# Kernel optimization log

Measured on AMD Instinct MI355X. Metric: run time of the kernel, lower is better.

Reference implementation:

```python
import jax, jax.numpy as jnp
import numpy as np

INF = 1e20


def setup_inputs() -> dict:
    key = jax.random.key(0)
    k1, k2, k3 = jax.random.split(key, 3)
    B, Q, M, F, D = 16, 64, 512, 16, 512
    return {
        "query_embed": jax.random.normal(k1, (B, Q, D), dtype=jnp.float32),
        "in_memory_embed": jax.random.normal(k2, (B, M, F, D), dtype=jnp.float32),
        "out_memory_embed": jax.random.normal(k3, (B, M, F, D), dtype=jnp.float32),
        "ctx_mask": jnp.ones((B, M, F), dtype=jnp.float32),
        "query_mask": jnp.ones((B, Q), dtype=jnp.float32),
    }


def reference(query_embed, in_memory_embed, out_memory_embed, ctx_mask, query_mask):
    # co-attention scores: [B, Q, M, F]
    attention = jnp.einsum("bqd,bmfd->bqmf", query_embed, in_memory_embed)
    # additive INF masking (torch: mask*att - (1-mask)*INF)
    cm = ctx_mask[:, None, :, :]            # [B,1,M,F]
    attention = cm * attention - (1.0 - cm) * INF
    qm = query_mask[:, :, None, None]       # [B,Q,1,1]
    attention = qm * attention - (1.0 - qm) * INF
    # NOTE: torch code computes a max-pool over Q for kb_feature_att but
    # immediately overwrites it with softmax of a ones/ctx mask -> dead code.
    mask = ctx_mask * 1.0 - (1.0 - ctx_mask) * INF        # [B,M,F]
    kb_feature_att = jax.nn.softmax(mask, axis=-1)        # [B,M,F]
    # weighted read over feature slots: [B,M,D]
    in_mem = jnp.einsum("bmf,bmfd->bmd", kb_feature_att, in_memory_embed)
    out_mem = out_memory_embed.sum(axis=2)                # [B,M,D]
    # max-pool over feature axis F -> [B,Q,M]
    att_qm = attention.max(axis=-1)
    probs = jax.nn.softmax(att_qm, axis=-1)               # over M
    new_query_embed = query_embed + jnp.einsum("bqm,bmd->bqd", probs, out_mem)
    probs2 = jax.nn.softmax(att_qm, axis=1)               # over Q
    in_mem = in_mem + jnp.einsum("bqm,bqd->bmd", probs2, new_query_embed)
    return (new_query_embed, in_mem, out_mem)
```

## Files before the change

kernel.cpp:

```cpp
#include <hip/hip_runtime.h>

#define INF_F 1e20f
#define B_ 16
#define Q_ 64
#define M_ 512
#define F_ 16
#define D_ 512

typedef __attribute__((ext_vector_type(8))) short short8v;
typedef __attribute__((ext_vector_type(4))) float f32x4;

static __device__ __forceinline__ float bits_f(unsigned u) { return __uint_as_float(u); }

static __device__ __forceinline__ void split4(float4 v, uint2& H, uint2& L) {
    unsigned hx = __float_as_uint(v.x) & 0xffff0000u, hy = __float_as_uint(v.y) & 0xffff0000u;
    unsigned hz = __float_as_uint(v.z) & 0xffff0000u, hw = __float_as_uint(v.w) & 0xffff0000u;
    H.x = (hx >> 16) | hy;
    H.y = (hz >> 16) | hw;
    L.x = (__float_as_uint(v.x - bits_f(hx)) >> 16) | (__float_as_uint(v.y - bits_f(hy)) & 0xffff0000u);
    L.y = (__float_as_uint(v.z - bits_f(hz)) >> 16) | (__float_as_uint(v.w - bits_f(hw)) & 0xffff0000u);
}

__global__ __launch_bounds__(256) void k_q_split(
    const float* __restrict__ q, short8v* __restrict__ qh, short8v* __restrict__ ql)
{
    int u = blockIdx.x * 256 + threadIdx.x;
    int row = u & 63, lg = (u >> 6) & 3, kc = (u >> 8) & 15, b = u >> 12;
    const float4* q4 = (const float4*)q;
    size_t s = (size_t)(b * 64 + row) * 128 + kc * 8 + lg * 2;
    float4 v0 = q4[s], v1 = q4[s + 1];
    uint2 H0, L0, H1, L1;
    split4(v0, H0, L0);
    split4(v1, H1, L1);
    uint4 H = make_uint4(H0.x, H0.y, H1.x, H1.y);
    uint4 L = make_uint4(L0.x, L0.y, L1.x, L1.y);
    *(uint4*)&qh[u] = H;
    *(uint4*)&ql[u] = L;
}

__global__ __launch_bounds__(256) void k_att_mfma(
    const short8v* __restrict__ qh, const short8v* __restrict__ ql,
    const float* __restrict__ in_mem, const float* __restrict__ out_mem,
    const float* __restrict__ ctx_mask, const float* __restrict__ query_mask,
    float* __restrict__ att_qm, float* __restrict__ in_mem_base,
    float* __restrict__ out_mem_sum)
{
    __shared__ __align__(16) short Mh[2][5120];
    __shared__ __align__(16) short Ml[2][5120];

    const int bid = blockIdx.x;
    const int b   = bid & 15;
    const int m0  = (bid >> 4) * 8;
    const int t   = threadIdx.x;
    const int w   = t >> 6;
    const int lane = t & 63;
    const int lr  = lane & 15;
    const int lg  = lane >> 4;
    const int r0  = t >> 3, c0 = t & 7;

    const int tt   = t & 127;
    const int msel = tt >> 4, col4 = (tt >> 1) & 7, half = tt & 1;
    const bool is_in = (t < 128);

    float wj[8];
    if (is_in) {
        const float* cm = ctx_mask + ((size_t)b * M_ + m0 + msel) * F_;
        float wv[16]; float mx = -INF_F;
        #pragma unroll
        for (int f = 0; f < 16; ++f) {
            float c = cm[f];
            float v = c - (1.0f - c) * INF_F;
            wv[f] = v; mx = fmaxf(mx, v);
        }
        float sum = 0.f;
        #pragma unroll
        for (int f = 0; f < 16; ++f) { wv[f] = __expf(wv[f] - mx); sum += wv[f]; }
        float inv = 1.0f / sum;
        #pragma unroll
        for (int j = 0; j < 8; ++j) wj[j] = wv[half * 8 + j] * inv;
    } else {
        #pragma unroll
        for (int j = 0; j < 8; ++j) wj[j] = 1.0f;
    }

    const float4* in4 = (const float4*)in_mem;
    const float4* ot4 = (const float4*)out_mem;
    const size_t mb    = (size_t)((b * M_ + m0) * F_) * 128;
    const float4* fsrc = is_in ? in4 : ot4;
    float4* fdst       = is_in ? (float4*)in_mem_base : (float4*)out_mem_sum;
    const size_t fbase = (size_t)((b * M_ + m0 + msel) * F_ + half * 8) * 128 + col4;
    const size_t fob   = (size_t)(b * M_ + m0 + msel) * 128 + col4;
    const int qbase0   = b * 16 * 256 + lg * 64 + lr;

    f32x4 acc[2][4];
    #pragma unroll
    for (int i = 0; i < 2; ++i)
        #pragma unroll
        for (int j = 0; j < 4; ++j) acc[i][j] = (f32x4){0, 0, 0, 0};

    float4 stg[4], fv[8];
    short8v qfh[4], qfl[4];

    #pragma unroll
    for (int i = 0; i < 4; ++i) stg[i] = in4[mb + (size_t)(r0 + i * 32) * 128 + c0];
    #pragma unroll
    for (int j = 0; j < 8; ++j) fv[j] = fsrc[fbase + (size_t)j * 128];
    #pragma unroll
    for (int tq = 0; tq < 4; ++tq) { qfh[tq] = qh[qbase0 + tq * 16]; qfl[tq] = ql[qbase0 + tq * 16]; }

#define BODY(kc_, bi_) do {                                                      \
                                              \
        _Pragma("unroll")                                                        \
        for (int i = 0; i < 4; ++i) {                                            \
            int r = r0 + i * 32;                                                 \
            uint2 H, L; split4(stg[i], H, L);                                    \
            int off = r * 40 + (((c0 >> 1) ^ ((r & 1) << 1)) << 3) + ((c0 & 1) << 2); \
            *(uint2*)&Mh[bi_][off] = H;                                          \
            *(uint2*)&Ml[bi_][off] = L;                                          \
        }                                                                        \
        if ((kc_) < 15) {                                                        \
            _Pragma("unroll")                                                    \
            for (int i = 0; i < 4; ++i)                                          \
                stg[i] = in4[mb + (size_t)(r0 + i * 32) * 128 + ((kc_) + 1) * 8 + c0]; \
        }                                                                        \
        asm volatile("s_waitcnt lgkmcnt(0)" ::: "memory");                       \
        __builtin_amdgcn_s_barrier();                                            \
                                                 \
        _Pragma("unroll")                                                        \
        for (int tm = 0; tm < 2; ++tm) {                                         \
            int row = (2 * w + tm) * 16 + lr;                                    \
            int off = row * 40 + ((lg ^ ((row & 1) << 1)) << 3);                 \
            short8v bh = *(const short8v*)&Mh[bi_][off];                         \
            short8v bl = *(const short8v*)&Ml[bi_][off];                         \
            _Pragma("unroll")                                                    \
            for (int tq = 0; tq < 4; ++tq) {                                     \
                acc[tm][tq] = __builtin_amdgcn_mfma_f32_16x16x32_bf16(qfh[tq], bh, acc[tm][tq], 0, 0, 0); \
                acc[tm][tq] = __builtin_amdgcn_mfma_f32_16x16x32_bf16(qfh[tq], bl, acc[tm][tq], 0, 0, 0); \
                acc[tm][tq] = __builtin_amdgcn_mfma_f32_16x16x32_bf16(qfl[tq], bh, acc[tm][tq], 0, 0, 0); \
            }                                                                    \
        }                                                                        \
        if ((kc_) < 15) {                                                        \
            int qb = qbase0 + ((kc_) + 1) * 256;                                 \
            _Pragma("unroll")                                                    \
            for (int tq = 0; tq < 4; ++tq) { qfh[tq] = qh[qb + tq * 16]; qfl[tq] = ql[qb + tq * 16]; } \
        }                                                                        \
                                                           \
        {                                                                        \
            float4 s = make_float4(0, 0, 0, 0);                                  \
            _Pragma("unroll")                                                    \
            for (int j = 0; j < 8; ++j) {                                        \
                s.x += wj[j] * fv[j].x; s.y += wj[j] * fv[j].y;                  \
                s.z += wj[j] * fv[j].z; s.w += wj[j] * fv[j].w;                  \
            }                                                                    \
            if ((kc_) < 15) {                                                    \
                _Pragma("unroll")                                                \
                for (int j = 0; j < 8; ++j)                                      \
                    fv[j] = fsrc[fbase + (size_t)j * 128 + ((kc_) + 1) * 8];     \
            }                                                                    \
            s.x += __shfl_xor(s.x, 1, 64); s.y += __shfl_xor(s.y, 1, 64);        \
            s.z += __shfl_xor(s.z, 1, 64); s.w += __shfl_xor(s.w, 1, 64);        \
            if (half == 0) fdst[fob + (kc_) * 8] = s;                            \
        }                                                                        \
    } while (0)

    for (int it = 0; it < 8; ++it) {
        int kc0 = 2 * it, kc1 = 2 * it + 1;
        BODY(kc0, 0);
        BODY(kc1, 1);
    }
#undef BODY

    #pragma unroll
    for (int tm = 0; tm < 2; ++tm) {
        int m = m0 + 2 * w + tm;
        float cmv = ctx_mask[((size_t)b * M_ + m) * F_ + lr];
        #pragma unroll
        for (int tq = 0; tq < 4; ++tq) {
            #pragma unroll
            for (int rg = 0; rg < 4; ++rg) {
                int q = tq * 16 + lg * 4 + rg;
                float qmv = query_mask[b * Q_ + q];
                float v = acc[tm][tq][rg];
                v = cmv * v - (1.0f - cmv) * INF_F;
                v = qmv * v - (1.0f - qmv) * INF_F;
                #pragma unroll
                for (int sh = 1; sh < 16; sh <<= 1) v = fmaxf(v, __shfl_xor(v, sh, 64));
                if (lr == 0)
                    att_qm[((size_t)b * Q_ + q) * M_ + m] = v;
            }
        }
    }
}

__global__ __launch_bounds__(128) void k_new_query(
    const float* __restrict__ att, const float* __restrict__ query,
    const float* __restrict__ out_sum, float* __restrict__ new_q)
{
    __shared__ float P[8][512];
    int bid = blockIdx.x;
    int b = bid & 15, qc = bid >> 4;
    int t = threadIdx.x;
    {
        int qi = t >> 4, l16 = t & 15;
        const float* row = att + ((size_t)b * Q_ + qc * 8 + qi) * M_;
        float vals[32]; float mx = -INF_F;
        #pragma unroll
        for (int i = 0; i < 32; ++i) { vals[i] = row[l16 + i * 16]; mx = fmaxf(mx, vals[i]); }
        #pragma unroll
        for (int s = 1; s < 16; s <<= 1) mx = fmaxf(mx, __shfl_xor(mx, s, 64));
        float sm = 0.f;
        #pragma unroll
        for (int i = 0; i < 32; ++i) { vals[i] = __expf(vals[i] - mx); sm += vals[i]; }
        #pragma unroll
        for (int s = 1; s < 16; s <<= 1) sm += __shfl_xor(sm, s, 64);
        float inv = 1.0f / sm;
        #pragma unroll
        for (int i = 0; i < 32; ++i) P[qi][l16 + i * 16] = vals[i] * inv;
    }
    __syncthreads();
    int c = t;
    const float4* o4 = (const float4*)out_sum + (size_t)b * M_ * 128 + c;
    const float4* q4 = (const float4*)query + ((size_t)b * Q_ + qc * 8) * 128 + c;
    float4 acc[8];
    #pragma unroll
    for (int qi = 0; qi < 8; ++qi) acc[qi] = q4[(size_t)qi * 128];
    for (int mm = 0; mm < M_; mm += 4) {
        float4 o0 = o4[(size_t)(mm + 0) * 128];
        float4 o1 = o4[(size_t)(mm + 1) * 128];
        float4 o2 = o4[(size_t)(mm + 2) * 128];
        float4 o3 = o4[(size_t)(mm + 3) * 128];
        #pragma unroll
        for (int qi = 0; qi < 8; ++qi) {
            float4 p = *(const float4*)&P[qi][mm];
            acc[qi].x += p.x * o0.x + p.y * o1.x + p.z * o2.x + p.w * o3.x;
            acc[qi].y += p.x * o0.y + p.y * o1.y + p.z * o2.y + p.w * o3.y;
            acc[qi].z += p.x * o0.z + p.y * o1.z + p.z * o2.z + p.w * o3.z;
            acc[qi].w += p.x * o0.w + p.y * o1.w + p.z * o2.w + p.w * o3.w;
        }
    }
    float4* n4 = (float4*)new_q + ((size_t)b * Q_ + qc * 8) * 128 + c;
    #pragma unroll
    for (int qi = 0; qi < 8; ++qi) n4[(size_t)qi * 128] = acc[qi];
}

__global__ __launch_bounds__(128) void k_in_mem(
    const float* __restrict__ att, const float* __restrict__ new_q,
    float* __restrict__ in_mem_io)
{
    __shared__ float P[8][64];
    int bid = blockIdx.x;
    int b = bid & 15, mc = bid >> 4;
    int m0 = mc * 8;
    int t = threadIdx.x;
    {
        int mi = t >> 4, l16 = t & 15;
        float v[4]; float mx = -INF_F;
        #pragma unroll
        for (int i = 0; i < 4; ++i) {
            v[i] = att[((size_t)b * Q_ + l16 + i * 16) * M_ + m0 + mi];
            mx = fmaxf(mx, v[i]);
        }
        #pragma unroll
        for (int s = 1; s < 16; s <<= 1) mx = fmaxf(mx, __shfl_xor(mx, s, 64));
        float sm = 0.f;
        #pragma unroll
        for (int i = 0; i < 4; ++i) { v[i] = __expf(v[i] - mx); sm += v[i]; }
        #pragma unroll
        for (int s = 1; s < 16; s <<= 1) sm += __shfl_xor(sm, s, 64);
        float inv = 1.0f / sm;
        #pragma unroll
        for (int i = 0; i < 4; ++i) P[mi][l16 + i * 16] = v[i] * inv;
    }
    __syncthreads();
    int c = t;
    float4* io = (float4*)in_mem_io + ((size_t)b * M_ + m0) * 128 + c;
    const float4* n4 = (const float4*)new_q + (size_t)b * Q_ * 128 + c;
    float4 acc[8];
    #pragma unroll
    for (int mi = 0; mi < 8; ++mi) acc[mi] = io[(size_t)mi * 128];
    for (int q = 0; q < Q_; q += 4) {
        float4 n0 = n4[(size_t)(q + 0) * 128];
        float4 n1 = n4[(size_t)(q + 1) * 128];
        float4 n2 = n4[(size_t)(q + 2) * 128];
        float4 n3 = n4[(size_t)(q + 3) * 128];
        #pragma unroll
        for (int mi = 0; mi < 8; ++mi) {
            float4 p = *(const float4*)&P[mi][q];
            acc[mi].x += p.x * n0.x + p.y * n1.x + p.z * n2.x + p.w * n3.x;
            acc[mi].y += p.x * n0.y + p.y * n1.y + p.z * n2.y + p.w * n3.y;
            acc[mi].z += p.x * n0.z + p.y * n1.z + p.z * n2.z + p.w * n3.z;
            acc[mi].w += p.x * n0.w + p.y * n1.w + p.z * n2.w + p.w * n3.w;
        }
    }
    #pragma unroll
    for (int mi = 0; mi < 8; ++mi) io[(size_t)mi * 128] = acc[mi];
}

extern "C" void kernel_launch(void* const* d_in, const int* in_sizes, int n_in,
                              void* d_out, int out_size, void* d_ws, size_t ws_size,
                              hipStream_t stream)
{
    const float* query      = (const float*)d_in[0];
    const float* in_mem     = (const float*)d_in[1];
    const float* out_mem    = (const float*)d_in[2];
    const float* ctx_mask   = (const float*)d_in[3];
    const float* query_mask = (const float*)d_in[4];

    float* out = (float*)d_out;
    float* new_q      = out;
    float* in_mem_out = out + (size_t)B_*Q_*D_;
    float* out_mem_o  = in_mem_out + (size_t)B_*M_*D_;

    float* ws       = (float*)d_ws;
    float* att_qm   = ws;
    short8v* qh     = (short8v*)(ws + (size_t)B_*Q_*M_);
    short8v* ql     = qh + 65536;

    hipLaunchKernelGGL(k_q_split, dim3(256), dim3(256), 0, stream, query, qh, ql);
    hipLaunchKernelGGL(k_att_mfma, dim3((M_/8) * B_), dim3(256), 0, stream,
                       qh, ql, in_mem, out_mem, ctx_mask, query_mask,
                       att_qm, in_mem_out, out_mem_o);
    hipLaunchKernelGGL(k_new_query, dim3(8 * B_), dim3(128), 0, stream,
                       att_qm, query, out_mem_o, new_q);
    hipLaunchKernelGGL(k_in_mem, dim3(64 * B_), dim3(128), 0, stream,
                       att_qm, new_q, in_mem_out);
}
```

Measured before the change: 249.6 us.

## Split attention MFMA and feature reductions into separate block roles without LDS

```diff
diff --git a/kernel.cpp b/kernel.cpp
--- a/kernel.cpp
+++ b/kernel.cpp
@@ -19,6 +19,12 @@
     H.y = (hz >> 16) | hw;
     L.x = (__float_as_uint(v.x - bits_f(hx)) >> 16) | (__float_as_uint(v.y - bits_f(hy)) & 0xffff0000u);
     L.y = (__float_as_uint(v.z - bits_f(hz)) >> 16) | (__float_as_uint(v.w - bits_f(hw)) & 0xffff0000u);
+}
+
+static __device__ __forceinline__ short8v mk8(uint2 a, uint2 b) {
+    union { uint4 u; short8v s; } r;
+    r.u = make_uint4(a.x, a.y, b.x, b.y);
+    return r.s;
 }
 
 __global__ __launch_bounds__(256) void k_q_split(
@@ -38,157 +44,145 @@
     *(uint4*)&ql[u] = L;
 }
 
-__global__ __launch_bounds__(256) void k_att_mfma(
-    const short8v* __restrict__ qh, const short8v* __restrict__ ql,
+__global__ __launch_bounds__(256, 4) void k_att_mfma(
+    const short8v* __restrict__ qhg, const short8v* __restrict__ qlg,
     const float* __restrict__ in_mem, const float* __restrict__ out_mem,
     const float* __restrict__ ctx_mask, const float* __restrict__ query_mask,
     float* __restrict__ att_qm, float* __restrict__ in_mem_base,
     float* __restrict__ out_mem_sum)
 {
-    __shared__ __align__(16) short Mh[2][5120];
-    __shared__ __align__(16) short Ml[2][5120];
-
     const int bid = blockIdx.x;
-    const int b   = bid & 15;
-    const int m0  = (bid >> 4) * 8;
-    const int t   = threadIdx.x;
-    const int w   = t >> 6;
-    const int lane = t & 63;
-    const int lr  = lane & 15;
-    const int lg  = lane >> 4;
-    const int r0  = t >> 3, c0 = t & 7;
-
-    const int tt   = t & 127;
-    const int msel = tt >> 4, col4 = (tt >> 1) & 7, half = tt & 1;
-    const bool is_in = (t < 128);
-
-    float wj[8];
-    if (is_in) {
-        const float* cm = ctx_mask + ((size_t)b * M_ + m0 + msel) * F_;
-        float wv[16]; float mx = -INF_F;
-        #pragma unroll
-        for (int f = 0; f < 16; ++f) {
-            float c = cm[f];
-            float v = c - (1.0f - c) * INF_F;
-            wv[f] = v; mx = fmaxf(mx, v);
-        }
-        float sum = 0.f;
-        #pragma unroll
-        for (int f = 0; f < 16; ++f) { wv[f] = __expf(wv[f] - mx); sum += wv[f]; }
-        float inv = 1.0f / sum;
-        #pragma unroll
-        for (int j = 0; j < 8; ++j) wj[j] = wv[half * 8 + j] * inv;
+    const int b    = bid & 15;
+    const int role = (bid >> 4) & 1;
+    const int m0   = (bid >> 5) * 8;
+    const int t    = threadIdx.x;
+
+    if (role == 0) {
+        const int w = t >> 6, lane = t & 63;
+        const int lr = lane & 15, lg = lane >> 4;
+        const float4* in4 = (const float4*)in_mem;
+        const size_t rb0 = (size_t)((b * M_ + m0 + 2 * w) * F_ + lr) * 128 + lg * 2;
+        const size_t rb1 = rb0 + (size_t)F_ * 128;
+        const int qb0 = b * 4096 + lg * 64 + lr;
+
+        f32x4 acc[2][4];
+        #pragma unroll
+        for (int i = 0; i < 2; ++i)
+            #pragma unroll
+            for (int j = 0; j < 4; ++j) acc[i][j] = (f32x4){0, 0, 0, 0};
+
+        float4 sc[4], sn[4];
+        sc[0] = in4[rb0]; sc[1] = in4[rb0 + 1];
+        sc[2] = in4[rb1]; sc[3] = in4[rb1 + 1];
+
+#define MBODY(kc_, cur, nxt) do {                                              \
+        if ((kc_) < 15) {                                                      \
+            size_t o = (size_t)((kc_) + 1) * 8;                                \
+            nxt[0] = in4[rb0 + o]; nxt[1] = in4[rb0 + o + 1];                  \
+            nxt[2] = in4[rb1 + o]; nxt[3] = in4[rb1 + o + 1];                  \
+        }                                                                      \
+        uint2 H0, L0, H1, L1;                                                  \
+        split4(cur[0], H0, L0); split4(cur[1], H1, L1);                        \
+        short8v bh0 = mk8(H0, H1), bl0 = mk8(L0, L1);                          \
+        split4(cur[2], H0, L0); split4(cur[3], H1, L1);                        \
+        short8v bh1 = mk8(H0, H1), bl1 = mk8(L0, L1);                          \
+        const int qb = qb0 + (kc_) * 256;                                      \
+        _Pragma("unroll")                                                      \
+        for (int tq = 0; tq < 4; ++tq) {                                       \
+            short8v ah = qhg[qb + tq * 16];                                    \
+            short8v al = qlg[qb + tq * 16];                                    \
+            acc[0][tq] = __builtin_amdgcn_mfma_f32_16x16x32_bf16(ah, bh0, acc[0][tq], 0, 0, 0); \
+            acc[0][tq] = __builtin_amdgcn_mfma_f32_16x16x32_bf16(ah, bl0, acc[0][tq], 0, 0, 0); \
+            acc[0][tq] = __builtin_amdgcn_mfma_f32_16x16x32_bf16(al, bh0, acc[0][tq], 0, 0, 0); \
+            acc[1][tq] = __builtin_amdgcn_mfma_f32_16x16x32_bf16(ah, bh1, acc[1][tq], 0, 0, 0); \
+            acc[1][tq] = __builtin_amdgcn_mfma_f32_16x16x32_bf16(ah, bl1, acc[1][tq], 0, 0, 0); \
+            acc[1][tq] = __builtin_amdgcn_mfma_f32_16x16x32_bf16(al, bh1, acc[1][tq], 0, 0, 0); \
+        }                                                                      \
+    } while (0)
+
+        for (int it = 0; it < 8; ++it) {
+            MBODY(2 * it, sc, sn);
+            MBODY(2 * it + 1, sn, sc);
+        }
+#undef MBODY
+
+        #pragma unroll
+        for (int tm = 0; tm < 2; ++tm) {
+            int m = m0 + 2 * w + tm;
+            float cmv = ctx_mask[((size_t)b * M_ + m) * F_ + lr];
+            #pragma unroll
+            for (int tq = 0; tq < 4; ++tq) {
+                #pragma unroll
+                for (int rg = 0; rg < 4; ++rg) {
+                    int q = tq * 16 + lg * 4 + rg;
+                    float qmv = query_mask[b * Q_ + q];
+                    float v = acc[tm][tq][rg];
+                    v = cmv * v - (1.0f - cmv) * INF_F;
+                    v = qmv * v - (1.0f - qmv) * INF_F;
+                    #pragma unroll
+                    for (int sh = 1; sh < 16; sh <<= 1) v = fmaxf(v, __shfl_xor(v, sh, 64));
+                    if (lr == 0)
+                        att_qm[((size_t)b * Q_ + q) * M_ + m] = v;
+                }
+            }
+        }
     } else {
-        #pragma unroll
-        for (int j = 0; j < 8; ++j) wj[j] = 1.0f;
-    }
-
-    const float4* in4 = (const float4*)in_mem;
-    const float4* ot4 = (const float4*)out_mem;
-    const size_t mb    = (size_t)((b * M_ + m0) * F_) * 128;
-    const float4* fsrc = is_in ? in4 : ot4;
-    float4* fdst       = is_in ? (float4*)in_mem_base : (float4*)out_mem_sum;
-    const size_t fbase = (size_t)((b * M_ + m0 + msel) * F_ + half * 8) * 128 + col4;
-    const size_t fob   = (size_t)(b * M_ + m0 + msel) * 128 + col4;
-    const int qbase0   = b * 16 * 256 + lg * 64 + lr;
-
-    f32x4 acc[2][4];
-    #pragma unroll
-    for (int i = 0; i < 2; ++i)
-        #pragma unroll
-        for (int j = 0; j < 4; ++j) acc[i][j] = (f32x4){0, 0, 0, 0};
-
-    float4 stg[4], fv[8];
-    short8v qfh[4], qfl[4];
-
-    #pragma unroll
-    for (int i = 0; i < 4; ++i) stg[i] = in4[mb + (size_t)(r0 + i * 32) * 128 + c0];
-    #pragma unroll
-    for (int j = 0; j < 8; ++j) fv[j] = fsrc[fbase + (size_t)j * 128];
-    #pragma unroll
-    for (int tq = 0; tq < 4; ++tq) { qfh[tq] = qh[qbase0 + tq * 16]; qfl[tq] = ql[qbase0 + tq * 16]; }
-
-#define BODY(kc_, bi_) do {                                                      \
-                                              \
-        _Pragma("unroll")                                                        \
-        for (int i = 0; i < 4; ++i) {                                            \
-            int r = r0 + i * 32;                                                 \
-            uint2 H, L; split4(stg[i], H, L);                                    \
-            int off = r * 40 + (((c0 >> 1) ^ ((r & 1) << 1)) << 3) + ((c0 & 1) << 2); \
-            *(uint2*)&Mh[bi_][off] = H;                                          \
-            *(uint2*)&Ml[bi_][off] = L;                                          \
-        }                                                                        \
-        if ((kc_) < 15) {                                                        \
-            _Pragma("unroll")                                                    \
-            for (int i = 0; i < 4; ++i)                                          \
-                stg[i] = in4[mb + (size_t)(r0 + i * 32) * 128 + ((kc_) + 1) * 8 + c0]; \
-        }                                                                        \
-        asm volatile("s_waitcnt lgkmcnt(0)" ::: "memory");                       \
-        __builtin_amdgcn_s_barrier();                                            \
-                                                 \
-        _Pragma("unroll")                                                        \
-        for (int tm = 0; tm < 2; ++tm) {                                         \
-            int row = (2 * w + tm) * 16 + lr;                                    \
-            int off = row * 40 + ((lg ^ ((row & 1) << 1)) << 3);                 \
-            short8v bh = *(const short8v*)&Mh[bi_][off];                         \
-            short8v bl = *(const short8v*)&Ml[bi_][off];                         \
-            _Pragma("unroll")                                                    \
-            for (int tq = 0; tq < 4; ++tq) {                                     \
-                acc[tm][tq] = __builtin_amdgcn_mfma_f32_16x16x32_bf16(qfh[tq], bh, acc[tm][tq], 0, 0, 0); \
-                acc[tm][tq] = __builtin_amdgcn_mfma_f32_16x16x32_bf16(qfh[tq], bl, acc[tm][tq], 0, 0, 0); \
-                acc[tm][tq] = __builtin_amdgcn_mfma_f32_16x16x32_bf16(qfl[tq], bh, acc[tm][tq], 0, 0, 0); \
-            }                                                                    \
-        }                                                                        \
-        if ((kc_) < 15) {                                                        \
-            int qb = qbase0 + ((kc_) + 1) * 256;                                 \
-            _Pragma("unroll")                                                    \
-            for (int tq = 0; tq < 4; ++tq) { qfh[tq] = qh[qb + tq * 16]; qfl[tq] = ql[qb + tq * 16]; } \
-        }                                                                        \
-                                                           \
-        {                                                                        \
-            float4 s = make_float4(0, 0, 0, 0);                                  \
-            _Pragma("unroll")                                                    \
-            for (int j = 0; j < 8; ++j) {                                        \
-                s.x += wj[j] * fv[j].x; s.y += wj[j] * fv[j].y;                  \
-                s.z += wj[j] * fv[j].z; s.w += wj[j] * fv[j].w;                  \
-            }                                                                    \
-            if ((kc_) < 15) {                                                    \
-                _Pragma("unroll")                                                \
-                for (int j = 0; j < 8; ++j)                                      \
-                    fv[j] = fsrc[fbase + (size_t)j * 128 + ((kc_) + 1) * 8];     \
-            }                                                                    \
-            s.x += __shfl_xor(s.x, 1, 64); s.y += __shfl_xor(s.y, 1, 64);        \
-            s.z += __shfl_xor(s.z, 1, 64); s.w += __shfl_xor(s.w, 1, 64);        \
-            if (half == 0) fdst[fob + (kc_) * 8] = s;                            \
-        }                                                                        \
+        const int th = t & 127;
+        const bool is_in = (t < 128);
+        const int msel = th >> 4, col4 = (th >> 1) & 7, half = th & 1;
+
+        float wj[8];
+        if (is_in) {
+            const float* cm = ctx_mask + ((size_t)b * M_ + m0 + msel) * F_;
+            float wv[16]; float mx = -INF_F;
+            #pragma unroll
+            for (int f = 0; f < 16; ++f) {
+                float c = cm[f];
+                float v = c - (1.0f - c) * INF_F;
+                wv[f] = v; mx = fmaxf(mx, v);
+            }
+            float sum = 0.f;
+            #pragma unroll
+            for (int f = 0; f < 16; ++f) { wv[f] = __expf(wv[f] - mx); sum += wv[f]; }
+            float inv = 1.0f / sum;
+            #pragma unroll
+            for (int j = 0; j < 8; ++j) wj[j] = wv[half * 8 + j] * inv;
+        } else {
+            #pragma unroll
+            for (int j = 0; j < 8; ++j) wj[j] = 1.0f;
+        }
+
+        const float4* fsrc = is_in ? (const float4*)in_mem : (const float4*)out_mem;
+        float4* fdst       = is_in ? (float4*)in_mem_base : (float4*)out_mem_sum;
+        const size_t fbase = (size_t)((b * M_ + m0 + msel) * F_ + half * 8) * 128 + col4;
+        const size_t fob   = (size_t)(b * M_ + m0 + msel) * 128 + col4;
+
+        float4 fa[8], fb[8];
+        #pragma unroll
+        for (int j = 0; j < 8; ++j) fa[j] = fsrc[fbase + (size_t)j * 128];
+
+#define FBODY(kc_, cur, nxt) do {                                              \
+        if ((kc_) < 15) {                                                      \
+            _Pragma("unroll")                                                  \
+            for (int j = 0; j < 8; ++j)                                        \
+                nxt[j] = fsrc[fbase + (size_t)j * 128 + ((kc_) + 1) * 8];      \
+        }                                                                      \
+        float4 s = make_float4(0, 0, 0, 0);                                    \
+        _Pragma("unroll")                                                      \
+        for (int j = 0; j < 8; ++j) {                                          \
+            s.x += wj[j] * cur[j].x; s.y += wj[j] * cur[j].y;                  \
+            s.z += wj[j] * cur[j].z; s.w += wj[j] * cur[j].w;                  \
+        }                                                                      \
+        s.x += __shfl_xor(s.x, 1, 64); s.y += __shfl_xor(s.y, 1, 64);          \
+        s.z += __shfl_xor(s.z, 1, 64); s.w += __shfl_xor(s.w, 1, 64);          \
+        if (half == 0) fdst[fob + (kc_) * 8] = s;                              \
     } while (0)
 
-    for (int it = 0; it < 8; ++it) {
-        int kc0 = 2 * it, kc1 = 2 * it + 1;
-        BODY(kc0, 0);
-        BODY(kc1, 1);
-    }
-#undef BODY
-
-    #pragma unroll
-    for (int tm = 0; tm < 2; ++tm) {
-        int m = m0 + 2 * w + tm;
-        float cmv = ctx_mask[((size_t)b * M_ + m) * F_ + lr];
-        #pragma unroll
-        for (int tq = 0; tq < 4; ++tq) {
-            #pragma unroll
-            for (int rg = 0; rg < 4; ++rg) {
-                int q = tq * 16 + lg * 4 + rg;
-                float qmv = query_mask[b * Q_ + q];
-                float v = acc[tm][tq][rg];
-                v = cmv * v - (1.0f - cmv) * INF_F;
-                v = qmv * v - (1.0f - qmv) * INF_F;
-                #pragma unroll
-                for (int sh = 1; sh < 16; sh <<= 1) v = fmaxf(v, __shfl_xor(v, sh, 64));
-                if (lr == 0)
-                    att_qm[((size_t)b * Q_ + q) * M_ + m] = v;
-            }
-        }
+        for (int it = 0; it < 8; ++it) {
+            FBODY(2 * it, fa, fb);
+            FBODY(2 * it + 1, fb, fa);
+        }
+#undef FBODY
     }
 }
 
@@ -317,7 +311,7 @@
     short8v* ql     = qh + 65536;
 
     hipLaunchKernelGGL(k_q_split, dim3(256), dim3(256), 0, stream, query, qh, ql);
-    hipLaunchKernelGGL(k_att_mfma, dim3((M_/8) * B_), dim3(256), 0, stream,
+    hipLaunchKernelGGL(k_att_mfma, dim3((M_/8) * B_ * 2), dim3(256), 0, stream,
                        qh, ql, in_mem, out_mem, ctx_mask, query_mask,
                        att_qm, in_mem_out, out_mem_o);
     hipLaunchKernelGGL(k_new_query, dim3(8 * B_), dim3(128), 0, stream,
```

After: 265.4 us. 6.3% more time.

## Fuse attention GEMM with weighted feature reductions and drop block barriers

Applied to the files above, without the earlier changes.

```diff
diff --git a/kernel.cpp b/kernel.cpp
--- a/kernel.cpp
+++ b/kernel.cpp
@@ -32,21 +32,19 @@
     uint2 H0, L0, H1, L1;
     split4(v0, H0, L0);
     split4(v1, H1, L1);
-    uint4 H = make_uint4(H0.x, H0.y, H1.x, H1.y);
-    uint4 L = make_uint4(L0.x, L0.y, L1.x, L1.y);
-    *(uint4*)&qh[u] = H;
-    *(uint4*)&ql[u] = L;
-}
-
-__global__ __launch_bounds__(256) void k_att_mfma(
-    const short8v* __restrict__ qh, const short8v* __restrict__ ql,
+    *(uint4*)&qh[u] = make_uint4(H0.x, H0.y, H1.x, H1.y);
+    *(uint4*)&ql[u] = make_uint4(L0.x, L0.y, L1.x, L1.y);
+}
+
+__global__ __launch_bounds__(256) void k_att_fused(
+    const short8v* __restrict__ qhg, const short8v* __restrict__ qlg,
     const float* __restrict__ in_mem, const float* __restrict__ out_mem,
     const float* __restrict__ ctx_mask, const float* __restrict__ query_mask,
     float* __restrict__ att_qm, float* __restrict__ in_mem_base,
     float* __restrict__ out_mem_sum)
 {
-    __shared__ __align__(16) short Mh[2][5120];
-    __shared__ __align__(16) short Ml[2][5120];
+    __shared__ __align__(16) short Mh[5120];
+    __shared__ __align__(16) short Ml[5120];
 
     const int bid = blockIdx.x;
     const int b   = bid & 15;
@@ -56,41 +54,33 @@
     const int lane = t & 63;
     const int lr  = lane & 15;
     const int lg  = lane >> 4;
-    const int r0  = t >> 3, c0 = t & 7;
-
-    const int tt   = t & 127;
-    const int msel = tt >> 4, col4 = (tt >> 1) & 7, half = tt & 1;
-    const bool is_in = (t < 128);
-
-    float wj[8];
-    if (is_in) {
-        const float* cm = ctx_mask + ((size_t)b * M_ + m0 + msel) * F_;
+    const int c   = lane & 7;
+    const int b0  = (lane >> 3) & 1;
+    const int mm  = 2 * w + b0;
+
+    float wj[4];
+    {
+        const float* cm = ctx_mask + ((size_t)b * M_ + m0 + mm) * F_;
         float wv[16]; float mx = -INF_F;
         #pragma unroll
         for (int f = 0; f < 16; ++f) {
-            float c = cm[f];
-            float v = c - (1.0f - c) * INF_F;
+            float cv = cm[f];
+            float v = cv - (1.0f - cv) * INF_F;
             wv[f] = v; mx = fmaxf(mx, v);
         }
-        float sum = 0.f;
-        #pragma unroll
-        for (int f = 0; f < 16; ++f) { wv[f] = __expf(wv[f] - mx); sum += wv[f]; }
-        float inv = 1.0f / sum;
-        #pragma unroll
-        for (int j = 0; j < 8; ++j) wj[j] = wv[half * 8 + j] * inv;
-    } else {
-        #pragma unroll
-        for (int j = 0; j < 8; ++j) wj[j] = 1.0f;
+        float s = 0.f;
+        #pragma unroll
+        for (int f = 0; f < 16; ++f) { wv[f] = __expf(wv[f] - mx); s += wv[f]; }
+        float inv = 1.0f / s;
+        #pragma unroll
+        for (int i = 0; i < 4; ++i) wj[i] = wv[lg * 4 + i] * inv;
     }
 
     const float4* in4 = (const float4*)in_mem;
     const float4* ot4 = (const float4*)out_mem;
-    const size_t mb    = (size_t)((b * M_ + m0) * F_) * 128;
-    const float4* fsrc = is_in ? in4 : ot4;
-    float4* fdst       = is_in ? (float4*)in_mem_base : (float4*)out_mem_sum;
-    const size_t fbase = (size_t)((b * M_ + m0 + msel) * F_ + half * 8) * 128 + col4;
-    const size_t fob   = (size_t)(b * M_ + m0 + msel) * 128 + col4;
-    const int qbase0   = b * 16 * 256 + lg * 64 + lr;
+    const int grow  = ((b * M_ + m0 + mm) * F_ + lg * 4) * 128 + c;
+    const int qb0   = b * 4096 + lg * 64 + lr;
+    const int obase = (b * M_ + m0 + mm) * 128 + c;
 
     f32x4 acc[2][4];
     #pragma unroll
@@ -98,77 +88,67 @@
         #pragma unroll
         for (int j = 0; j < 4; ++j) acc[i][j] = (f32x4){0, 0, 0, 0};
 
-    float4 stg[4], fv[8];
-    short8v qfh[4], qfl[4];
-
-    #pragma unroll
-    for (int i = 0; i < 4; ++i) stg[i] = in4[mb + (size_t)(r0 + i * 32) * 128 + c0];
-    #pragma unroll
-    for (int j = 0; j < 8; ++j) fv[j] = fsrc[fbase + (size_t)j * 128];
-    #pragma unroll
-    for (int tq = 0; tq < 4; ++tq) { qfh[tq] = qh[qbase0 + tq * 16]; qfl[tq] = ql[qbase0 + tq * 16]; }
-
-#define BODY(kc_, bi_) do {                                                      \
-                                              \
-        _Pragma("unroll")                                                        \
-        for (int i = 0; i < 4; ++i) {                                            \
-            int r = r0 + i * 32;                                                 \
-            uint2 H, L; split4(stg[i], H, L);                                    \
-            int off = r * 40 + (((c0 >> 1) ^ ((r & 1) << 1)) << 3) + ((c0 & 1) << 2); \
-            *(uint2*)&Mh[bi_][off] = H;                                          \
-            *(uint2*)&Ml[bi_][off] = L;                                          \
-        }                                                                        \
-        if ((kc_) < 15) {                                                        \
-            _Pragma("unroll")                                                    \
-            for (int i = 0; i < 4; ++i)                                          \
-                stg[i] = in4[mb + (size_t)(r0 + i * 32) * 128 + ((kc_) + 1) * 8 + c0]; \
-        }                                                                        \
-        asm volatile("s_waitcnt lgkmcnt(0)" ::: "memory");                       \
-        __builtin_amdgcn_s_barrier();                                            \
-                                                 \
-        _Pragma("unroll")                                                        \
-        for (int tm = 0; tm < 2; ++tm) {                                         \
-            int row = (2 * w + tm) * 16 + lr;                                    \
-            int off = row * 40 + ((lg ^ ((row & 1) << 1)) << 3);                 \
-            short8v bh = *(const short8v*)&Mh[bi_][off];                         \
-            short8v bl = *(const short8v*)&Ml[bi_][off];                         \
-            _Pragma("unroll")                                                    \
-            for (int tq = 0; tq < 4; ++tq) {                                     \
-                acc[tm][tq] = __builtin_amdgcn_mfma_f32_16x16x32_bf16(qfh[tq], bh, acc[tm][tq], 0, 0, 0); \
-                acc[tm][tq] = __builtin_amdgcn_mfma_f32_16x16x32_bf16(qfh[tq], bl, acc[tm][tq], 0, 0, 0); \
-                acc[tm][tq] = __builtin_amdgcn_mfma_f32_16x16x32_bf16(qfl[tq], bh, acc[tm][tq], 0, 0, 0); \
-            }                                                                    \
-        }                                                                        \
-        if ((kc_) < 15) {                                                        \
-            int qb = qbase0 + ((kc_) + 1) * 256;                                 \
-            _Pragma("unroll")                                                    \
-            for (int tq = 0; tq < 4; ++tq) { qfh[tq] = qh[qb + tq * 16]; qfl[tq] = ql[qb + tq * 16]; } \
-        }                                                                        \
-                                                           \
-        {                                                                        \
-            float4 s = make_float4(0, 0, 0, 0);                                  \
-            _Pragma("unroll")                                                    \
-            for (int j = 0; j < 8; ++j) {                                        \
-                s.x += wj[j] * fv[j].x; s.y += wj[j] * fv[j].y;                  \
-                s.z += wj[j] * fv[j].z; s.w += wj[j] * fv[j].w;                  \
-            }                                                                    \
-            if ((kc_) < 15) {                                                    \
-                _Pragma("unroll")                                                \
-                for (int j = 0; j < 8; ++j)                                      \
-                    fv[j] = fsrc[fbase + (size_t)j * 128 + ((kc_) + 1) * 8];     \
-            }                                                                    \
-            s.x += __shfl_xor(s.x, 1, 64); s.y += __shfl_xor(s.y, 1, 64);        \
-            s.z += __shfl_xor(s.z, 1, 64); s.w += __shfl_xor(s.w, 1, 64);        \
-            if (half == 0) fdst[fob + (kc_) * 8] = s;                            \
-        }                                                                        \
-    } while (0)
-
-    for (int it = 0; it < 8; ++it) {
-        int kc0 = 2 * it, kc1 = 2 * it + 1;
-        BODY(kc0, 0);
-        BODY(kc1, 1);
-    }
-#undef BODY
+    float4 si[2][4], so[2][4];
+    short8v qf[2][8];
+
+    #pragma unroll
+    for (int i = 0; i < 4; ++i) { si[0][i] = in4[grow + i * 128]; so[0][i] = ot4[grow + i * 128]; }
+    #pragma unroll
+    for (int tq = 0; tq < 4; ++tq) { qf[0][tq] = qhg[qb0 + tq * 16]; qf[0][4 + tq] = qlg[qb0 + tq * 16]; }
+
+    #pragma unroll
+    for (int kc = 0; kc < 16; ++kc) {
+        const int cur = kc & 1, nxt = cur ^ 1;
+        if (kc < 15) {
+            const int go = grow + (kc + 1) * 8;
+            #pragma unroll
+            for (int i = 0; i < 4; ++i) { si[nxt][i] = in4[go + i * 128]; so[nxt][i] = ot4[go + i * 128]; }
+            const int qb = qb0 + (kc + 1) * 256;
+            #pragma unroll
+            for (int tq = 0; tq < 4; ++tq) { qf[nxt][tq] = qhg[qb + tq * 16]; qf[nxt][4 + tq] = qlg[qb + tq * 16]; }
+        }
+        float4 sin_ = make_float4(0, 0, 0, 0), sot_ = make_float4(0, 0, 0, 0);
+        #pragma unroll
+        for (int i = 0; i < 4; ++i) {
+            float4 a = si[cur][i];
+            uint2 H, L; split4(a, H, L);
+            const int rl = mm * 16 + lg * 4 + i;
+            const int off = rl * 40 + (((c >> 1) ^ ((rl & 1) << 1)) << 3) + ((c & 1) << 2);
+            *(uint2*)&Mh[off] = H;
+            *(uint2*)&Ml[off] = L;
+            sin_.x += wj[i] * a.x; sin_.y += wj[i] * a.y;
+            sin_.z += wj[i] * a.z; sin_.w += wj[i] * a.w;
+            float4 o = so[cur][i];
+            sot_.x += o.x; sot_.y += o.y; sot_.z += o.z; sot_.w += o.w;
+        }
+        #pragma unroll
+        for (int sh = 16; sh <= 32; sh <<= 1) {
+            sin_.x += __shfl_xor(sin_.x, sh, 64); sin_.y += __shfl_xor(sin_.y, sh, 64);
+            sin_.z += __shfl_xor(sin_.z, sh, 64); sin_.w += __shfl_xor(sin_.w, sh, 64);
+            sot_.x += __shfl_xor(sot_.x, sh, 64); sot_.y += __shfl_xor(sot_.y, sh, 64);
+            sot_.z += __shfl_xor(sot_.z, sh, 64); sot_.w += __shfl_xor(sot_.w, sh, 64);
+        }
+        if (lg == 0) {
+            ((float4*)in_mem_base)[obase + kc * 8] = sin_;
+            ((float4*)out_mem_sum)[obase + kc * 8] = sot_;
+        }
+        #pragma unroll
+        for (int tm = 0; tm < 2; ++tm) {
+            const int row = (2 * w + tm) * 16 + lr;
+            const int off = row * 40 + ((lg ^ ((row & 1) << 1)) << 3);
+            short8v bh = *(const short8v*)&Mh[off];
+            short8v bl = *(const short8v*)&Ml[off];
+            __builtin_amdgcn_s_setprio(1);
+            #pragma unroll
+            for (int tq = 0; tq < 4; ++tq) {
+                short8v ah = qf[cur][tq], al = qf[cur][4 + tq];
+                acc[tm][tq] = __builtin_amdgcn_mfma_f32_16x16x32_bf16(ah, bh, acc[tm][tq], 0, 0, 0);
+                acc[tm][tq] = __builtin_amdgcn_mfma_f32_16x16x32_bf16(ah, bl, acc[tm][tq], 0, 0, 0);
+                acc[tm][tq] = __builtin_amdgcn_mfma_f32_16x16x32_bf16(al, bh, acc[tm][tq], 0, 0, 0);
+            }
+            __builtin_amdgcn_s_setprio(0);
+        }
+    }
 
     #pragma unroll
     for (int tm = 0; tm < 2; ++tm) {
@@ -317,7 +297,7 @@
     short8v* ql     = qh + 65536;
 
     hipLaunchKernelGGL(k_q_split, dim3(256), dim3(256), 0, stream, query, qh, ql);
-    hipLaunchKernelGGL(k_att_mfma, dim3((M_/8) * B_), dim3(256), 0, stream,
+    hipLaunchKernelGGL(k_att_fused, dim3((M_/8) * B_), dim3(256), 0, stream,
                        qh, ql, in_mem, out_mem, ctx_mask, query_mask,
                        att_qm, in_mem_out, out_mem_o);
     hipLaunchKernelGGL(k_new_query, dim3(8 * B_), dim3(128), 0, stream,
```

After: 243.5 us. -2.5%, faster.
